# Kernel tuning notes

Measured on AMD Instinct MI355X. Metric: run time of the kernel, lower is better.

Reference implementation:

```python
import jax, jax.numpy as jnp
import numpy as np

K, D, O, B = 65536, 256, 256, 1024

def setup_inputs() -> dict:
    key = jax.random.key(0)
    k1, k2, k3 = jax.random.split(key, 3)
    return {
        "x": jax.random.normal(k1, (B, D), dtype=jnp.float32),
        "mean": jax.random.normal(k2, (K, D), dtype=jnp.float32),
        "stddev": jnp.ones((K, D), dtype=jnp.float32),
        "outputs": jax.random.normal(k3, (K, O), dtype=jnp.float32),
        "top_k": 32,
    }

def reference(x, mean, stddev, outputs, top_k):
    # Joint Gaussian log-prob summed over feature dim, computed without the
    # [B, K, D] broadcast torch materializes. Expanding sum_d ((x-mu)/sigma)^2
    # gives three GEMM-shaped terms.
    d = x.shape[-1]
    inv_var = 1.0 / (stddev * stddev)                      # [K, D]
    quad = ((x * x) @ inv_var.T                            # [B, K]
            - 2.0 * (x @ (mean * inv_var).T)
            + jnp.sum(mean * mean * inv_var, axis=-1))
    log_norm = jnp.sum(jnp.log(stddev), axis=-1) + 0.5 * d * jnp.log(2.0 * jnp.pi)
    joint_lp = -0.5 * quad - log_norm                      # [B, K]
    top_lp, top_idx = jax.lax.top_k(joint_lp, top_k)       # [B, top_k]
    weights = jax.nn.softmax(top_lp, axis=-1)              # [B, top_k]
    gathered = outputs[top_idx]                            # [B, top_k, O]
    return jnp.einsum('bko,bk->bo', gathered, weights)     # [B, O]
```

## Files before the change

kernel.cpp:

```cpp
#include <hip/hip_runtime.h>
#include <stdint.h>

#define KCOMP 65536
#define DDIM  256
#define ODIM  256
#define BROWS 1024
#define NCB   512
#define NBLK  512
#define LOG2PI_TERM 235.2482645f

typedef float f32x4 __attribute__((ext_vector_type(4)));
typedef __bf16 bf16x8 __attribute__((ext_vector_type(8)));
typedef unsigned int u32;
typedef unsigned long long u64;
typedef unsigned short u16;

typedef __attribute__((address_space(1))) const u32 gconst_u32;
typedef __attribute__((address_space(3))) u32 lds_u32;

__device__ __forceinline__ u16 f2bf(float f) {
  u32 b = __float_as_uint(f);
  b += 0x7FFFu + ((b >> 16) & 1u);
  return (u16)(b >> 16);
}
__device__ __forceinline__ u32 fkey(float f) {
  u32 b = __float_as_uint(f);
  return b ^ ((b >> 31) ? 0xFFFFFFFFu : 0x80000000u);
}

#define DPP_ROR1 0x121
#define DPP_ROR2 0x122
#define DPP_ROR4 0x124
#define DPP_ROR8 0x128

#define WS_A     0
#define WS_KEY   (1u << 20)

__global__ void prep_A(const float* __restrict__ x, u16* __restrict__ A) {
  int l = threadIdx.x & 63;
  int wv = threadIdx.x >> 6;
  int t = blockIdx.x;
  int row = t * 16 + (l & 15);
  for (int u = 0; u < 4; ++u) {
    int cc = wv * 4 + u;
    int d0 = cc * 16 + ((l >> 4) << 2);
    float4 xv = *(const float4*)(x + (size_t)row * DDIM + d0);
    float xs[4] = {xv.x, xv.y, xv.z, xv.w};
    uint4 v;
    u32 wds[4];
    for (int e = 0; e < 4; ++e)
      wds[e] = (u32)f2bf(xs[e] * xs[e]) | ((u32)f2bf(-2.0f * xs[e]) << 16);
    v.x = wds[0]; v.y = wds[1]; v.z = wds[2]; v.w = wds[3];
    *(uint4*)(A + ((size_t)(t * 16 + cc) * 64 + l) * 8) = v;
  }
}

__global__ __launch_bounds__(256, 2)
void main_gemm(const u16* __restrict__ A_ws, const float* __restrict__ mean,
               const float* __restrict__ stdd, u32* __restrict__ ckey) {
  __shared__ __align__(16) char lds_raw[66560];
  __shared__ u32 wsel[2][32][9];
  int tid = threadIdx.x, l = tid & 63, w = tid >> 6;
  int nb = blockIdx.x;
  int g0 = nb * 8 + w * 2;
  int p = l & 15, q = l >> 4;

  u32 kidv[8];
#pragma unroll
  for (int gs = 0; gs < 2; ++gs)
#pragma unroll
    for (int i = 0; i < 4; ++i)
      kidv[gs * 4 + i] = (u32)(w * 32 + gs * 16 + q * 4 + i);

  bf16x8 wf[2][16];
  float myc[2];
  f32x4 mycv[2];
  {
    u32* scr = (u32*)(lds_raw + w * 16640);
#pragma unroll
    for (int gs = 0; gs < 2; ++gs) {
      int comp = (g0 + gs) * 16 + p;
      const float* mrow = mean + (size_t)comp * DDIM + q * 64;
      const float* srow = stdd + (size_t)comp * DDIM + q * 64;
      float gsum = 0.f;
#pragma unroll
      for (int i = 0; i < 16; ++i) {
        float4 m4 = *(const float4*)(mrow + 4 * i);
        float4 s4 = *(const float4*)(srow + 4 * i);
        float ms[4] = {m4.x, m4.y, m4.z, m4.w};
        float ss[4] = {s4.x, s4.y, s4.z, s4.w};
        u32 wd[4];
#pragma unroll
        for (int e = 0; e < 4; ++e) {
          float iv = __builtin_amdgcn_rcpf(ss[e] * ss[e]);
          float miv = ms[e] * iv;
          wd[e] = (u32)f2bf(-0.5f * iv) | ((u32)f2bf(-0.5f * miv) << 16);
          gsum -= 0.5f * ms[e] * miv + __logf(ss[e]);
        }
        uint4 v; v.x = wd[0]; v.y = wd[1]; v.z = wd[2]; v.w = wd[3];
        *(uint4*)(scr + p * 260 + q * 64 + i * 4) = v;
      }
      gsum += __shfl_xor(gsum, 16);
      gsum += __shfl_xor(gsum, 32);
      myc[gs] = gsum - LOG2PI_TERM;
#pragma unroll
      for (int cc = 0; cc < 16; ++cc)
        wf[gs][cc] = *(const bf16x8*)(scr + p * 260 + cc * 16 + q * 4);
    }
#pragma unroll
    for (int gs = 0; gs < 2; ++gs)
#pragma unroll
      for (int i = 0; i < 4; ++i)
        mycv[gs][i] = __shfl(myc[gs], q * 4 + i);
  }
  __syncthreads();

#define ASHP(B, CELL) (lds_raw + ((size_t)(B) * 32 + (CELL)) * 1024)

#define ISSUE(S, B)                                                           \
  {                                                                           \
    _Pragma("unroll")                                                         \
    for (int u = 0; u < 8; ++u) {                                             \
      int cell = w * 8 + u;                                                   \
      const u16* gsrc = A_ws +                                                \
        ((size_t)((S) * 2 + (cell >> 4)) * 16 + (cell & 15)) * 512            \
        + (size_t)l * 8;                                                      \
      __builtin_amdgcn_global_load_lds((gconst_u32*)gsrc,                     \
          (lds_u32*)ASHP(B, cell), 16, 0, 0);                                 \
    }                                                                         \
  }

#define MERGE_EMIT(ST, B)                                                     \
  {                                                                           \
    int r = tid;                                                              \
    u32 top[4] = {~0u, ~0u, ~0u, ~0u};                                        \
    _Pragma("unroll")                                                         \
    for (int j = 0; j < 8; ++j) {                                             \
      u32 key = wsel[B][r][j];                                                \
      if (key < top[3]) {                                                     \
        top[3] = key;                                                         \
        for (int z = 3; z > 0 && top[z] < top[z - 1]; --z) {                  \
          u32 tt = top[z]; top[z] = top[z - 1]; top[z - 1] = tt;              \
        }                                                                     \
      }                                                                       \
    }                                                                         \
    int rowg = (ST) * 32 + r;                                                 \
    uint4 ov; ov.x = ~top[0]; ov.y = ~top[1]; ov.z = ~top[2]; ov.w = ~top[3]; \
    *(uint4*)&ckey[((size_t)rowg * NCB + nb) * 4] = ov;                       \
  }

  ISSUE(0, 0)
  for (int s = 0; s < 32; ++s) {
    int pb = s & 1;
    __syncthreads();
    if (s < 31) ISSUE(s + 1, pb ^ 1)
    if (s > 0 && tid < 32) MERGE_EMIT(s - 1, pb ^ 1)

    f32x4 ac[2][2];
#pragma unroll
    for (int t = 0; t < 2; ++t) {
      ac[t][0] = mycv[0];
      ac[t][1] = mycv[1];
    }
#pragma unroll
    for (int cc = 0; cc < 16; ++cc) {
      bf16x8 a0 = *(const bf16x8*)(ASHP(pb, cc) + (size_t)l * 16);
      bf16x8 a1 = *(const bf16x8*)(ASHP(pb, 16 + cc) + (size_t)l * 16);
      ac[0][0] = __builtin_amdgcn_mfma_f32_16x16x32_bf16(wf[0][cc], a0, ac[0][0], 0, 0, 0);
      ac[0][1] = __builtin_amdgcn_mfma_f32_16x16x32_bf16(wf[1][cc], a0, ac[0][1], 0, 0, 0);
      ac[1][0] = __builtin_amdgcn_mfma_f32_16x16x32_bf16(wf[0][cc], a1, ac[1][0], 0, 0, 0);
      ac[1][1] = __builtin_amdgcn_mfma_f32_16x16x32_bf16(wf[1][cc], a1, ac[1][1], 0, 0, 0);
    }

#define UMIN(a, b) ((a) < (b) ? (a) : (b))
#define UMAX(a, b) ((a) < (b) ? (b) : (a))
#pragma unroll
    for (int t = 0; t < 2; ++t) {
      u32 k0 = (__float_as_uint(ac[t][0][0]) & 0xFFFFFF00u) | kidv[0];
      u32 k1 = (__float_as_uint(ac[t][0][1]) & 0xFFFFFF00u) | kidv[1];
      u32 k2 = (__float_as_uint(ac[t][0][2]) & 0xFFFFFF00u) | kidv[2];
      u32 k3 = (__float_as_uint(ac[t][0][3]) & 0xFFFFFF00u) | kidv[3];
      u32 k4 = (__float_as_uint(ac[t][1][0]) & 0xFFFFFF00u) | kidv[4];
      u32 k5 = (__float_as_uint(ac[t][1][1]) & 0xFFFFFF00u) | kidv[5];
      u32 k6 = (__float_as_uint(ac[t][1][2]) & 0xFFFFFF00u) | kidv[6];
      u32 k7 = (__float_as_uint(ac[t][1][3]) & 0xFFFFFF00u) | kidv[7];
      u32 l0 = UMIN(k0, k1), h0 = UMAX(k0, k1);
      u32 l1 = UMIN(k2, k3), h1 = UMAX(k2, k3);
      u32 l2 = UMIN(k4, k5), h2 = UMAX(k4, k5);
      u32 l3 = UMIN(k6, k7), h3 = UMAX(k6, k7);
      u32 A1 = UMIN(l0, l1), A2 = UMIN(UMAX(l0, l1), UMIN(h0, h1));
      u32 B1 = UMIN(l2, l3), B2 = UMIN(UMAX(l2, l3), UMIN(h2, h3));
      u32 m1 = UMIN(A1, B1), m2 = UMIN(UMAX(A1, B1), UMIN(A2, B2));
      {
        u32 o1 = (u32)__shfl_xor((int)m1, 16);
        u32 o2 = (u32)__shfl_xor((int)m2, 16);
        u32 lo = UMIN(m1, o1), hi = UMAX(m1, o1), mn = UMIN(m2, o2);
        m1 = lo; m2 = UMIN(hi, mn);
      }
      {
        u32 o1 = (u32)__shfl_xor((int)m1, 32);
        u32 o2 = (u32)__shfl_xor((int)m2, 32);
        u32 lo = UMIN(m1, o1), hi = UMAX(m1, o1), mn = UMIN(m2, o2);
        m1 = lo; m2 = UMIN(hi, mn);
      }
      if (q == 0) {
        int r = t * 16 + p;
        wsel[pb][r][w * 2] = m1;
        wsel[pb][r][w * 2 + 1] = m2;
      }
    }
#undef UMIN
#undef UMAX
  }
  __syncthreads();
  if (tid < 32) MERGE_EMIT(31, 1)
#undef ISSUE
#undef MERGE_EMIT
#undef ASHP
}

__global__ __launch_bounds__(256)
void finalize(const float* __restrict__ x, const float* __restrict__ mean,
              const float* __restrict__ stdd, const float* __restrict__ outs,
              const u32* __restrict__ ckey, float* __restrict__ out) {
  __shared__ u32 cksh[2048];
  __shared__ float xr[256];
  __shared__ float part[256];
  __shared__ int selk[64];
  __shared__ float ew[32];
  __shared__ int kf[32];
  __shared__ float invs_sh;
  int tid = threadIdx.x, l = tid & 63, v = tid >> 6;
  int row = blockIdx.x;

  for (int i = tid; i < 2048; i += 256)
    cksh[i] = ckey[(size_t)row * 2048 + i];
  xr[tid] = x[(size_t)row * DDIM + tid];
  __syncthreads();

#define REDUCE_MAX(m)                                                         \
  {                                                                           \
    u32 o;                                                                    \
    o = (u32)__builtin_amdgcn_mov_dpp((int)m, DPP_ROR1, 0xf, 0xf, false);     \
    m = m > o ? m : o;                                                        \
    o = (u32)__builtin_amdgcn_mov_dpp((int)m, DPP_ROR2, 0xf, 0xf, false);     \
    m = m > o ? m : o;                                                        \
    o = (u32)__builtin_amdgcn_mov_dpp((int)m, DPP_ROR4, 0xf, 0xf, false);     \
    m = m > o ? m : o;                                                        \
    o = (u32)__builtin_amdgcn_mov_dpp((int)m, DPP_ROR8, 0xf, 0xf, false);     \
    m = m > o ? m : o;                                                        \
    o = (u32)__shfl_xor((int)m, 16); m = m > o ? m : o;                       \
    o = (u32)__shfl_xor((int)m, 32); m = m > o ? m : o;                       \
  }

  {
    u32 ext[8];
#pragma unroll
    for (int i = 0; i < 8; ++i) {
      int j = v * 512 + i * 64 + l;
      ext[i] = (cksh[j] & 0xFFFFFE00u) | ((u32)l << 3) | (u32)i;
    }
#define CSW(a, b) { if (ext[a] < ext[b]) { u32 t = ext[a]; ext[a] = ext[b]; ext[b] = t; } }
    CSW(0,1) CSW(2,3) CSW(4,5) CSW(6,7)
    CSW(0,2) CSW(1,3) CSW(4,6) CSW(5,7)
    CSW(1,2) CSW(5,6)
    CSW(0,4) CSW(1,5) CSW(2,6) CSW(3,7)
    CSW(2,4) CSW(3,5)
    CSW(1,2) CSW(3,4) CSW(5,6)
#undef CSW
    for (int it = 0; it < 16; ++it) {
      u32 m = ext[0];
      REDUCE_MAX(m)
      if (m == ext[0]) {
#pragma unroll
        for (int z = 0; z < 7; ++z) ext[z] = ext[z + 1];
        ext[7] = 0;
      }
      if (l == 0) {
        int wl = (int)((m >> 3) & 63u), wi = (int)(m & 7u);
        int j = v * 512 + wi * 64 + wl;
        selk[v * 16 + it] = (int)((u32)(j >> 2) * 128u + (~cksh[j] & 0x7Fu));
      }
    }
  }
  __syncthreads();

  {
    int j = tid >> 2, qq = tid & 3;
    int k = selk[j];
    const float* mr = mean + (size_t)k * DDIM + qq * 64;
    const float* sr = stdd + (size_t)k * DDIM + qq * 64;
    float s2 = 0.f, ls = 0.f;
    for (int i = 0; i < 16; ++i) {
      float4 m4 = *(const float4*)(mr + 4 * i);
      float4 s4 = *(const float4*)(sr + 4 * i);
      float4 x4 = *(const float4*)(&xr[qq * 64 + 4 * i]);
      { float is = 1.f / s4.x; float df = (x4.x - m4.x) * is; s2 += df * df; ls += __logf(s4.x); }
      { float is = 1.f / s4.y; float df = (x4.y - m4.y) * is; s2 += df * df; ls += __logf(s4.y); }
      { float is = 1.f / s4.z; float df = (x4.z - m4.z) * is; s2 += df * df; ls += __logf(s4.z); }
      { float is = 1.f / s4.w; float df = (x4.w - m4.w) * is; s2 += df * df; ls += __logf(s4.w); }
    }
    part[tid] = -0.5f * s2 - ls;
  }
  __syncthreads();

  if (tid < 64) {
    float lp0 = part[l * 4] + part[l * 4 + 1] + part[l * 4 + 2] +
                part[l * 4 + 3] - LOG2PI_TERM;
    u32 ext = (fkey(lp0) & 0xFFFFFFC0u) | (u32)l;
    float maxlp = 0.f, ssum = 0.f;
    for (int it = 0; it < 32; ++it) {
      u32 m = ext;
      REDUCE_MAX(m)
      int j = (int)(m & 63u);
      u32 vb = m & 0xFFFFFFC0u;
      vb ^= (vb >> 31) ? 0x80000000u : 0xFFFFFFFFu;
      float lp = __uint_as_float(vb);
      if (it == 0) maxlp = lp;
      float e = __expf(lp - maxlp);
      ssum += e;
      if (l == 0) { ew[it] = e; kf[it] = selk[j]; }
      if (j == l) ext = 0;
    }
    if (l == 0) invs_sh = 1.0f / ssum;
  }
  __syncthreads();
#undef REDUCE_MAX

  {
    float a = 0.f;
    for (int i = 0; i < 32; ++i)
      a += ew[i] * outs[(size_t)kf[i] * ODIM + tid];
    out[(size_t)row * ODIM + tid] = a * invs_sh;
  }
}

extern "C" void kernel_launch(void* const* d_in, const int* in_sizes, int n_in,
                              void* d_out, int out_size, void* d_ws, size_t ws_size,
                              hipStream_t stream) {
  const float* x = (const float*)d_in[0];
  const float* mean = (const float*)d_in[1];
  const float* stdd = (const float*)d_in[2];
  const float* outs = (const float*)d_in[3];
  char* ws = (char*)d_ws;
  u16* A_ws = (u16*)(ws + WS_A);
  u32* ckey = (u32*)(ws + WS_KEY);

  prep_A<<<64, 256, 0, stream>>>(x, A_ws);
  main_gemm<<<NBLK, 256, 0, stream>>>(A_ws, mean, stdd, ckey);
  finalize<<<BROWS, 256, 0, stream>>>(x, mean, stdd, outs, ckey,
                                      (float*)d_out);
}
```

Baseline: 387.8 us.

## Split main GEMM across 8 waves, one component group per wave, raise priority

Result: faster. 379.7 us (-2.1%).

```diff
diff --git a/kernel.cpp b/kernel.cpp
--- a/kernel.cpp
+++ b/kernel.cpp
@@ -55,36 +55,31 @@
   }
 }
 
-__global__ __launch_bounds__(256, 2)
+__global__ __launch_bounds__(512, 4)
 void main_gemm(const u16* __restrict__ A_ws, const float* __restrict__ mean,
                const float* __restrict__ stdd, u32* __restrict__ ckey) {
   __shared__ __align__(16) char lds_raw[66560];
-  __shared__ u32 wsel[2][32][9];
+  __shared__ u32 wsel[2][32][17];
   int tid = threadIdx.x, l = tid & 63, w = tid >> 6;
   int nb = blockIdx.x;
-  int g0 = nb * 8 + w * 2;
   int p = l & 15, q = l >> 4;
 
-  u32 kidv[8];
-#pragma unroll
-  for (int gs = 0; gs < 2; ++gs)
-#pragma unroll
-    for (int i = 0; i < 4; ++i)
-      kidv[gs * 4 + i] = (u32)(w * 32 + gs * 16 + q * 4 + i);
-
-  bf16x8 wf[2][16];
-  float myc[2];
-  f32x4 mycv[2];
+  u32 kid0 = (u32)(w * 16 + q * 4);
+
+  bf16x8 wf[16];
+  float myc0;
+  f32x4 mycv;
   {
-    u32* scr = (u32*)(lds_raw + w * 16640);
-#pragma unroll
-    for (int gs = 0; gs < 2; ++gs) {
-      int comp = (g0 + gs) * 16 + p;
-      const float* mrow = mean + (size_t)comp * DDIM + q * 64;
-      const float* srow = stdd + (size_t)comp * DDIM + q * 64;
+    u32* scr = (u32*)(lds_raw + w * 8320);
+    int p8 = l & 7, q8 = l >> 3;
+#pragma unroll
+    for (int rr = 0; rr < 2; ++rr) {
+      int comp = (nb * 8 + w) * 16 + rr * 8 + p8;
+      const float* mrow = mean + (size_t)comp * DDIM + q8 * 32;
+      const float* srow = stdd + (size_t)comp * DDIM + q8 * 32;
       float gsum = 0.f;
 #pragma unroll
-      for (int i = 0; i < 16; ++i) {
+      for (int i = 0; i < 8; ++i) {
         float4 m4 = *(const float4*)(mrow + 4 * i);
         float4 s4 = *(const float4*)(srow + 4 * i);
         float ms[4] = {m4.x, m4.y, m4.z, m4.w};
@@ -98,20 +93,21 @@
           gsum -= 0.5f * ms[e] * miv + __logf(ss[e]);
         }
         uint4 v; v.x = wd[0]; v.y = wd[1]; v.z = wd[2]; v.w = wd[3];
-        *(uint4*)(scr + p * 260 + q * 64 + i * 4) = v;
-      }
+        *(uint4*)(scr + p8 * 260 + q8 * 32 + i * 4) = v;
+      }
+      gsum += __shfl_xor(gsum, 8);
       gsum += __shfl_xor(gsum, 16);
       gsum += __shfl_xor(gsum, 32);
-      myc[gs] = gsum - LOG2PI_TERM;
-#pragma unroll
-      for (int cc = 0; cc < 16; ++cc)
-        wf[gs][cc] = *(const bf16x8*)(scr + p * 260 + cc * 16 + q * 4);
-    }
-#pragma unroll
-    for (int gs = 0; gs < 2; ++gs)
-#pragma unroll
-      for (int i = 0; i < 4; ++i)
-        mycv[gs][i] = __shfl(myc[gs], q * 4 + i);
+      if ((p >> 3) == rr) {
+        myc0 = gsum - LOG2PI_TERM;
+#pragma unroll
+        for (int cc = 0; cc < 16; ++cc)
+          wf[cc] = *(const bf16x8*)(scr + (p & 7) * 260 + cc * 16 + q * 4);
+      }
+    }
+#pragma unroll
+    for (int i = 0; i < 4; ++i)
+      mycv[i] = __shfl(myc0, q * 4 + i);
   }
   __syncthreads();
 
@@ -120,8 +116,8 @@
 #define ISSUE(S, B)                                                           \
   {                                                                           \
     _Pragma("unroll")                                                         \
-    for (int u = 0; u < 8; ++u) {                                             \
-      int cell = w * 8 + u;                                                   \
+    for (int u = 0; u < 4; ++u) {                                             \
+      int cell = w * 4 + u;                                                   \
       const u16* gsrc = A_ws +                                                \
         ((size_t)((S) * 2 + (cell >> 4)) * 16 + (cell & 15)) * 512            \
         + (size_t)l * 8;                                                      \
@@ -135,7 +131,7 @@
     int r = tid;                                                              \
     u32 top[4] = {~0u, ~0u, ~0u, ~0u};                                        \
     _Pragma("unroll")                                                         \
-    for (int j = 0; j < 8; ++j) {                                             \
+    for (int j = 0; j < 16; ++j) {                                            \
       u32 key = wsel[B][r][j];                                                \
       if (key < top[3]) {                                                     \
         top[3] = key;                                                         \
@@ -156,41 +152,30 @@
     if (s < 31) ISSUE(s + 1, pb ^ 1)
     if (s > 0 && tid < 32) MERGE_EMIT(s - 1, pb ^ 1)
 
-    f32x4 ac[2][2];
-#pragma unroll
-    for (int t = 0; t < 2; ++t) {
-      ac[t][0] = mycv[0];
-      ac[t][1] = mycv[1];
-    }
+    f32x4 ac[2];
+    ac[0] = mycv;
+    ac[1] = mycv;
+    __builtin_amdgcn_s_setprio(1);
 #pragma unroll
     for (int cc = 0; cc < 16; ++cc) {
       bf16x8 a0 = *(const bf16x8*)(ASHP(pb, cc) + (size_t)l * 16);
       bf16x8 a1 = *(const bf16x8*)(ASHP(pb, 16 + cc) + (size_t)l * 16);
-      ac[0][0] = __builtin_amdgcn_mfma_f32_16x16x32_bf16(wf[0][cc], a0, ac[0][0], 0, 0, 0);
-      ac[0][1] = __builtin_amdgcn_mfma_f32_16x16x32_bf16(wf[1][cc], a0, ac[0][1], 0, 0, 0);
-      ac[1][0] = __builtin_amdgcn_mfma_f32_16x16x32_bf16(wf[0][cc], a1, ac[1][0], 0, 0, 0);
-      ac[1][1] = __builtin_amdgcn_mfma_f32_16x16x32_bf16(wf[1][cc], a1, ac[1][1], 0, 0, 0);
-    }
+      ac[0] = __builtin_amdgcn_mfma_f32_16x16x32_bf16(wf[cc], a0, ac[0], 0, 0, 0);
+      ac[1] = __builtin_amdgcn_mfma_f32_16x16x32_bf16(wf[cc], a1, ac[1], 0, 0, 0);
+    }
+    __builtin_amdgcn_s_setprio(0);
 
 #define UMIN(a, b) ((a) < (b) ? (a) : (b))
 #define UMAX(a, b) ((a) < (b) ? (b) : (a))
 #pragma unroll
     for (int t = 0; t < 2; ++t) {
-      u32 k0 = (__float_as_uint(ac[t][0][0]) & 0xFFFFFF00u) | kidv[0];
-      u32 k1 = (__float_as_uint(ac[t][0][1]) & 0xFFFFFF00u) | kidv[1];
-      u32 k2 = (__float_as_uint(ac[t][0][2]) & 0xFFFFFF00u) | kidv[2];
-      u32 k3 = (__float_as_uint(ac[t][0][3]) & 0xFFFFFF00u) | kidv[3];
-      u32 k4 = (__float_as_uint(ac[t][1][0]) & 0xFFFFFF00u) | kidv[4];
-      u32 k5 = (__float_as_uint(ac[t][1][1]) & 0xFFFFFF00u) | kidv[5];
-      u32 k6 = (__float_as_uint(ac[t][1][2]) & 0xFFFFFF00u) | kidv[6];
-      u32 k7 = (__float_as_uint(ac[t][1][3]) & 0xFFFFFF00u) | kidv[7];
+      u32 k0 = (__float_as_uint(ac[t][0]) & 0xFFFFFF00u) | (kid0 + 0);
+      u32 k1 = (__float_as_uint(ac[t][1]) & 0xFFFFFF00u) | (kid0 + 1);
+      u32 k2 = (__float_as_uint(ac[t][2]) & 0xFFFFFF00u) | (kid0 + 2);
+      u32 k3 = (__float_as_uint(ac[t][3]) & 0xFFFFFF00u) | (kid0 + 3);
       u32 l0 = UMIN(k0, k1), h0 = UMAX(k0, k1);
       u32 l1 = UMIN(k2, k3), h1 = UMAX(k2, k3);
-      u32 l2 = UMIN(k4, k5), h2 = UMAX(k4, k5);
-      u32 l3 = UMIN(k6, k7), h3 = UMAX(k6, k7);
-      u32 A1 = UMIN(l0, l1), A2 = UMIN(UMAX(l0, l1), UMIN(h0, h1));
-      u32 B1 = UMIN(l2, l3), B2 = UMIN(UMAX(l2, l3), UMIN(h2, h3));
-      u32 m1 = UMIN(A1, B1), m2 = UMIN(UMAX(A1, B1), UMIN(A2, B2));
+      u32 m1 = UMIN(l0, l1), m2 = UMIN(UMAX(l0, l1), UMIN(h0, h1));
       {
         u32 o1 = (u32)__shfl_xor((int)m1, 16);
         u32 o2 = (u32)__shfl_xor((int)m2, 16);
@@ -347,7 +332,7 @@
   u32* ckey = (u32*)(ws + WS_KEY);
 
   prep_A<<<64, 256, 0, stream>>>(x, A_ws);
-  main_gemm<<<NBLK, 256, 0, stream>>>(A_ws, mean, stdd, ckey);
+  main_gemm<<<NBLK, 512, 0, stream>>>(A_ws, mean, stdd, ckey);
   finalize<<<BROWS, 256, 0, stream>>>(x, mean, stdd, outs, ckey,
                                       (float*)d_out);
 }
```
